# Kernel tuning notes

Hardware: AMD Instinct MI355X
Metric: run time of the kernel (lower is better)

## Reference

```python
import jax, jax.numpy as jnp
import numpy as np

S = 256      # pair sequence length (multiple of 32 -> no padding needed)
C = 128      # pair hidden dim
H = 4        # n_heads
D = 32       # head_dim
EPS = 1e-5
ENDING = False


def setup_inputs() -> dict:
    key = jax.random.key(0)
    ks = jax.random.split(key, 10)
    s = 0.02
    return {
        "x": jax.random.normal(ks[0], (1, S, S, C), dtype=jnp.float32),
        "ln_w": jnp.ones((C,), dtype=jnp.float32),
        "ln_b": jnp.zeros((C,), dtype=jnp.float32),
        "w_bias": jax.random.normal(ks[1], (H, C), dtype=jnp.float32) * s,   # linear.weight
        "w_q": jax.random.normal(ks[2], (H * D, C), dtype=jnp.float32) * s,  # linear_q.weight
        "w_k": jax.random.normal(ks[3], (H * D, C), dtype=jnp.float32) * s,
        "w_v": jax.random.normal(ks[4], (H * D, C), dtype=jnp.float32) * s,
        "w_g": jax.random.normal(ks[5], (H * D, C), dtype=jnp.float32) * s,  # linear_g.weight
        "w_o": jax.random.normal(ks[6], (C, H * D), dtype=jnp.float32) * s,  # linear_o.weight
    }


def reference(x, ln_w, ln_b, w_bias, w_q, w_k, w_v, w_g, w_o):
    h = x[0]  # [S, S, C]
    if ENDING:
        h = jnp.transpose(h, (1, 0, 2))
    # LayerNorm over channel dim
    mu = jnp.mean(h, axis=-1, keepdims=True)
    var = jnp.mean(jnp.square(h - mu), axis=-1, keepdims=True)
    h = (h - mu) * jax.lax.rsqrt(var + EPS) * ln_w + ln_b

    # pair-derived additive bias: [H, S, S], broadcast over the row (batch) dim
    tri_bias = jnp.einsum("ijc,hc->hij", h, w_bias)

    # per-head Q/K/V: weights are [H*D, C] with head-major rows
    wq = w_q.reshape(H, D, C)
    wk = w_k.reshape(H, D, C)
    wv = w_v.reshape(H, D, C)
    q = jnp.einsum("ijc,hdc->hijd", h, wq)  # [H, S(row), S(seq), D]
    k = jnp.einsum("ijc,hdc->hijd", h, wk)
    v = jnp.einsum("ijc,hdc->hijd", h, wv)

    scale = D ** -0.5
    # scores[h, i, j, k] = scale * q[h,i,j]\cdot k[h,i,k] + bias[h, j, k]
    scores = jnp.einsum("hijd,hikd->hijk", q, k) * scale + tri_bias[:, None, :, :]
    attn = jax.nn.softmax(scores, axis=-1)
    o = jnp.einsum("hijk,hikd->hijd", attn, v)          # [H, S, S, D]
    o = jnp.transpose(o, (1, 2, 0, 3)).reshape(S, S, H * D)

    # sigmoid gating and output projection
    g = jax.nn.sigmoid(jnp.einsum("ijc,ec->ije", h, w_g))
    out = jnp.einsum("ije,ce->ijc", o * g, w_o)          # [S, S, C]
    if ENDING:
        out = jnp.transpose(out, (1, 0, 2))
    return out[None]  # [1, S, S, C]
```

## Files before the change

kernel.cpp:

```cpp
#include <hip/hip_runtime.h>
#include <hip/hip_bf16.h>
#include <math.h>

#define SS 256
#define CC 128
#define NH 4
#define HD 32
#define M_TOT (SS*SS)
#define HEAD_STRIDE (M_TOT*HD)
#define PSTR 72
#define SCALE 0.17677669529663687f
#define QSCL 0.25507602861154995f
#define LOG2E 1.4426950408889634f

typedef short short8 __attribute__((ext_vector_type(8)));
typedef float f32x4 __attribute__((ext_vector_type(4)));
typedef unsigned short ushort_t;

static __device__ __forceinline__ unsigned int f2bf(float f) {
  unsigned int u = __builtin_bit_cast(unsigned int, f);
  u += 0x7fffu + ((u >> 16) & 1u);
  return u >> 16;
}
static __device__ __forceinline__ float bf2f(unsigned short b) {
  unsigned int u = ((unsigned int)b) << 16;
  return __builtin_bit_cast(float, u);
}

static __device__ __forceinline__ void async_copy16(const void* g, void* l) {
  __builtin_amdgcn_global_load_lds(
      (const __attribute__((address_space(1))) unsigned int*)g,
      (__attribute__((address_space(3))) unsigned int*)l, 16, 0, 0);
}

__global__ __launch_bounds__(256) void ln_kernel(
    const float* __restrict__ x, const float* __restrict__ ln_w,
    const float* __restrict__ ln_b, ushort_t* __restrict__ hbf) {
  int t = threadIdx.x;
  int row = blockIdx.x*8 + (t >> 5);
  int l = t & 31;
  float4 v = *(const float4*)&x[(size_t)row*CC + l*4];
  float s  = v.x + v.y + v.z + v.w;
  float s2 = v.x*v.x + v.y*v.y + v.z*v.z + v.w*v.w;
  #pragma unroll
  for (int o = 16; o > 0; o >>= 1) {
    s  += __shfl_xor(s, o);
    s2 += __shfl_xor(s2, o);
  }
  float mu  = s * (1.0f/CC);
  float var = s2 * (1.0f/CC) - mu*mu;
  float r = rsqrtf(var + 1e-5f);
  float4 w4 = *(const float4*)&ln_w[l*4];
  float4 b4 = *(const float4*)&ln_b[l*4];
  ushort4 o4;
  o4.x = (ushort_t)f2bf((v.x - mu) * r * w4.x + b4.x);
  o4.y = (ushort_t)f2bf((v.y - mu) * r * w4.y + b4.y);
  o4.z = (ushort_t)f2bf((v.z - mu) * r * w4.z + b4.z);
  o4.w = (ushort_t)f2bf((v.w - mu) * r * w4.w + b4.w);
  *(ushort4*)&hbf[(size_t)row*CC + l*4] = o4;
}

__global__ __launch_bounds__(256) void pack_w(
    const float* __restrict__ wq, const float* __restrict__ wk,
    const float* __restrict__ wv, const float* __restrict__ wg,
    const float* __restrict__ wb, const float* __restrict__ wo,
    ushort_t* __restrict__ wcomb, ushort_t* __restrict__ wbias,
    ushort_t* __restrict__ wobf) {
  int idx = blockIdx.x*256 + threadIdx.x;
  if (idx >= 656*128) return;
  int n = idx >> 7, kk = idx & 127;
  if (n < 512) {
    float val;
    if (n < 128)      val = wq[n*128 + kk];
    else if (n < 256) val = wk[(n-128)*128 + kk];
    else if (n < 384) val = wv[(n-256)*128 + kk];
    else              val = wg[(n-384)*128 + kk];
    wcomb[idx] = (ushort_t)f2bf(val);
  } else if (n < 528) {
    int r = n - 512;
    wbias[r*128 + kk] = (r < NH) ? (ushort_t)f2bf(wb[r*128 + kk] * LOG2E) : (ushort_t)0;
  } else {
    int r = n - 528;
    wobf[r*128 + kk] = (ushort_t)f2bf(wo[r*128 + kk]);
  }
}

__global__ __launch_bounds__(256, 3) void proj_mfma(
    const ushort_t* __restrict__ hbf, const ushort_t* __restrict__ wcomb,
    const ushort_t* __restrict__ wbias,
    ushort_t* __restrict__ qb, ushort_t* __restrict__ kb,
    ushort_t* __restrict__ vb, ushort_t* __restrict__ gbf,
    float* __restrict__ biasF) {
  __shared__ ushort_t Bsh[128*128];
  int mbase = blockIdx.x * 128;
  int sec = blockIdx.y;
  int tid = threadIdx.x;
  int wvi = tid >> 6, lane = tid & 63;
  int quad = lane >> 4, l15 = lane & 15;

  {
    int lrow4 = lane >> 4;
    int cl = lane & 15;
    #pragma unroll
    for (int t = 0; t < 8; t++) {
      int inst = wvi*8 + t;
      int row = inst*4 + lrow4;
      int gc = cl ^ (row & 7);
      async_copy16(wcomb + (size_t)(sec*128 + row)*128 + gc*8, Bsh + inst*512);
    }
  }
  __syncthreads();

  int wrow = (wvi >> 1) * 64, wcol = (wvi & 1) * 64;
  const f32x4 fz = {0.f,0.f,0.f,0.f};
  f32x4 acc[4][4];
  #pragma unroll
  for (int a = 0; a < 4; a++)
    #pragma unroll
    for (int b = 0; b < 4; b++) acc[a][b] = fz;

  #pragma unroll
  for (int s = 0; s < 4; s++) {
    short8 Af[4], Bf[4];
    #pragma unroll
    for (int f = 0; f < 4; f++) {
      int ra = mbase + wrow + f*16 + l15;
      Af[f] = *(const short8*)&hbf[(size_t)ra*128 + s*32 + quad*8];
      int rb = wcol + f*16 + l15;
      Bf[f] = *(const short8*)&Bsh[rb*128 + (((s*4+quad) ^ (rb&7)) << 3)];
    }
    #pragma unroll
    for (int mi = 0; mi < 4; mi++)
      #pragma unroll
      for (int ni = 0; ni < 4; ni++)
        acc[mi][ni] = __builtin_amdgcn_mfma_f32_16x16x32_bf16(Af[mi], Bf[ni], acc[mi][ni], 0, 0, 0);
  }

  #pragma unroll
  for (int mi = 0; mi < 4; mi++) {
    #pragma unroll
    for (int r = 0; r < 4; r++) {
      int m = mbase + wrow + mi*16 + quad*4 + r;
      #pragma unroll
      for (int ni = 0; ni < 4; ni++) {
        int n = wcol + ni*16 + l15;
        float v = acc[mi][ni][r];
        if (sec == 0) {
          qb[(size_t)(n>>5)*HEAD_STRIDE + (size_t)m*HD + (n&31)] = (ushort_t)f2bf(v * QSCL);
        } else if (sec == 1) {
          kb[(size_t)(n>>5)*HEAD_STRIDE + (size_t)m*HD + (n&31)] = (ushort_t)f2bf(v);
        } else if (sec == 2) {
          vb[(size_t)(n>>5)*HEAD_STRIDE + (size_t)m*HD + (n&31)] = (ushort_t)f2bf(v);
        } else {
          gbf[(size_t)m*CC + n] = (ushort_t)f2bf(1.0f/(1.0f + __expf(-v)));
        }
      }
    }
  }

  if (sec == 0) {
    short8 wbF[4];
    #pragma unroll
    for (int s = 0; s < 4; s++)
      wbF[s] = *(const short8*)&wbias[l15*128 + s*32 + quad*8];
    #pragma unroll
    for (int t2 = 0; t2 < 2; t2++) {
      int f2 = wvi*2 + t2;
      f32x4 bacc = fz;
      #pragma unroll
      for (int s = 0; s < 4; s++) {
        short8 Af = *(const short8*)&hbf[(size_t)(mbase + f2*16 + l15)*128 + s*32 + quad*8];
        bacc = __builtin_amdgcn_mfma_f32_16x16x32_bf16(wbF[s], Af, bacc, 0, 0, 0);
      }
      if (quad == 0) {
        int m = mbase + f2*16 + l15;
        int ji = m >> 8, ki = m & 255;
        int jt = ji >> 4, q2 = (ji >> 2) & 3, rg = ji & 3;
        int kt = ki >> 4, lf = ki & 15;
        #pragma unroll
        for (int r = 0; r < 4; r++)
          biasF[(size_t)(((r*16 + jt)*16 + kt) << 8) + (q2*16 + lf)*4 + rg] = bacc[r];
      }
    }
  }
}

__global__ __launch_bounds__(256, 3) void attn_mfma(
    const ushort_t* __restrict__ qb, const ushort_t* __restrict__ kb,
    const ushort_t* __restrict__ vb, const float* __restrict__ biasF,
    const ushort_t* __restrict__ gbf, ushort_t* __restrict__ ogated) {
  __shared__ ushort_t Vt[32*256];
  __shared__ ushort_t Pb[4*64*PSTR];
  int i = blockIdx.x, hh = blockIdx.y;
  int tid = threadIdx.x;
  int wvi = tid >> 6, lane = tid & 63;
  int quad = lane >> 4, l15 = lane & 15;

  {
    const ushort_t* vrow = vb + ((size_t)hh*M_TOT + (size_t)i*SS + tid) * HD;
    const uint4* v4 = (const uint4*)vrow;
    int cs = tid >> 3, ce = tid & 7;
    #pragma unroll
    for (int c = 0; c < 4; c++) {
      uint4 r = v4[c];
      unsigned int u[4] = {r.x, r.y, r.z, r.w};
      #pragma unroll
      for (int w = 0; w < 4; w++) {
        int d = c*8 + w*2;
        Vt[d*256     + ((cs ^ (d&7))     << 3) + ce] = (ushort_t)(u[w] & 0xffffu);
        Vt[(d+1)*256 + ((cs ^ ((d+1)&7)) << 3) + ce] = (ushort_t)(u[w] >> 16);
      }
    }
  }

  const ushort_t* qbase = qb + ((size_t)hh*M_TOT + (size_t)i*SS + wvi*64) * HD;
  short8 Qf[4];
  #pragma unroll
  for (int a = 0; a < 4; a++)
    Qf[a] = *(const short8*)(qbase + (a*16 + l15)*HD + quad*8);

  const ushort_t* kbp = kb + ((size_t)hh*M_TOT + (size_t)i*SS) * HD;
  const float* bb = biasF + (size_t)(hh*16 + wvi*4) * 4096;

  const f32x4 fz = {0.f, 0.f, 0.f, 0.f};
  f32x4 Oa[4][2];
  #pragma unroll
  for (int a = 0; a < 4; a++) { Oa[a][0] = fz; Oa[a][1] = fz; }
  float lsum[4][4] = {};

  ushort_t* pw = Pb + wvi*64*PSTR;

  __syncthreads();

  #pragma unroll
  for (int it = 0; it < 4; it++) {
    #pragma unroll
    for (int b = 0; b < 4; b++) {
      int kt = it*4 + b;
      short8 Kf = *(const short8*)(kbp + (kt*16 + l15)*HD + quad*8);
      #pragma unroll
      for (int a = 0; a < 4; a++) {
        float4 bt = *(const float4*)(bb + (size_t)((a*16 + kt) << 8) + lane*4);
        f32x4 bias4 = {bt.x, bt.y, bt.z, bt.w};
        f32x4 S = __builtin_amdgcn_mfma_f32_16x16x32_bf16(Qf[a], Kf, bias4, 0, 0, 0);
        float p0 = __builtin_amdgcn_exp2f(S[0]);
        float p1 = __builtin_amdgcn_exp2f(S[1]);
        float p2 = __builtin_amdgcn_exp2f(S[2]);
        float p3 = __builtin_amdgcn_exp2f(S[3]);
        lsum[a][0] += p0; lsum[a][1] += p1; lsum[a][2] += p2; lsum[a][3] += p3;
        ushort_t* pwa = pw + (a*16 + quad*4)*PSTR + b*16 + l15;
        pwa[0*PSTR] = (ushort_t)f2bf(p0);
        pwa[1*PSTR] = (ushort_t)f2bf(p1);
        pwa[2*PSTR] = (ushort_t)f2bf(p2);
        pwa[3*PSTR] = (ushort_t)f2bf(p3);
      }
    }
    #pragma unroll
    for (int kk = 0; kk < 2; kk++) {
      int cb = it*8 + kk*4;
      int sw = ((cb + quad) ^ (l15 & 7)) << 3;
      short8 Vf0 = *(const short8*)&Vt[l15*256 + sw];
      short8 Vf1 = *(const short8*)&Vt[(16 + l15)*256 + sw];
      #pragma unroll
      for (int a = 0; a < 4; a++) {
        short8 Pf = *(const short8*)&pw[(a*16 + l15)*PSTR + kk*32 + quad*8];
        Oa[a][0] = __builtin_amdgcn_mfma_f32_16x16x32_bf16(Pf, Vf0, Oa[a][0], 0, 0, 0);
        Oa[a][1] = __builtin_amdgcn_mfma_f32_16x16x32_bf16(Pf, Vf1, Oa[a][1], 0, 0, 0);
      }
    }
  }

  float linv[4][4];
  #pragma unroll
  for (int a = 0; a < 4; a++) {
    #pragma unroll
    for (int r = 0; r < 4; r++) {
      float v = lsum[a][r];
      v += __shfl_xor(v, 1);
      v += __shfl_xor(v, 2);
      v += __shfl_xor(v, 4);
      v += __shfl_xor(v, 8);
      linv[a][r] = 1.0f / v;
    }
  }
  const ushort_t* gp = gbf + ((size_t)i*SS + wvi*64)*CC + hh*HD;
  ushort_t* ob = ogated + ((size_t)i*SS + wvi*64)*CC + hh*HD;
  #pragma unroll
  for (int a = 0; a < 4; a++) {
    #pragma unroll
    for (int r = 0; r < 4; r++) {
      int row = (a*16 + quad*4 + r) * CC;
      float g0 = bf2f(gp[row + l15]);
      float g1 = bf2f(gp[row + 16 + l15]);
      ob[row + l15]      = (ushort_t)f2bf(Oa[a][0][r] * linv[a][r] * g0);
      ob[row + 16 + l15] = (ushort_t)f2bf(Oa[a][1][r] * linv[a][r] * g1);
    }
  }
}

__global__ __launch_bounds__(256, 3) void out_mfma(
    const ushort_t* __restrict__ ogated, const ushort_t* __restrict__ wobf,
    float* __restrict__ out) {
  __shared__ ushort_t Bsh[128*128];
  int mbase = blockIdx.x * 128;
  int tid = threadIdx.x;
  int wvi = tid >> 6, lane = tid & 63;
  int quad = lane >> 4, l15 = lane & 15;

  {
    int lrow4 = lane >> 4;
    int cl = lane & 15;
    #pragma unroll
    for (int t = 0; t < 8; t++) {
      int inst = wvi*8 + t;
      int row = inst*4 + lrow4;
      int gc = cl ^ (row & 7);
      async_copy16(wobf + (size_t)row*128 + gc*8, Bsh + inst*512);
    }
  }
  __syncthreads();

  int wrow = (wvi >> 1) * 64, wcol = (wvi & 1) * 64;
  const f32x4 fz = {0.f,0.f,0.f,0.f};
  f32x4 acc[4][4];
  #pragma unroll
  for (int a = 0; a < 4; a++)
    #pragma unroll
    for (int b = 0; b < 4; b++) acc[a][b] = fz;

  #pragma unroll
  for (int s = 0; s < 4; s++) {
    short8 Af[4], Bf[4];
    #pragma unroll
    for (int f = 0; f < 4; f++) {
      int ra = mbase + wrow + f*16 + l15;
      Af[f] = *(const short8*)&ogated[(size_t)ra*128 + s*32 + quad*8];
      int rb = wcol + f*16 + l15;
      Bf[f] = *(const short8*)&Bsh[rb*128 + (((s*4+quad) ^ (rb&7)) << 3)];
    }
    #pragma unroll
    for (int mi = 0; mi < 4; mi++)
      #pragma unroll
      for (int ni = 0; ni < 4; ni++)
        acc[mi][ni] = __builtin_amdgcn_mfma_f32_16x16x32_bf16(Af[mi], Bf[ni], acc[mi][ni], 0, 0, 0);
  }

  #pragma unroll
  for (int mi = 0; mi < 4; mi++) {
    #pragma unroll
    for (int r = 0; r < 4; r++) {
      int m = mbase + wrow + mi*16 + quad*4 + r;
      #pragma unroll
      for (int ni = 0; ni < 4; ni++) {
        int n = wcol + ni*16 + l15;
        out[(size_t)m*CC + n] = acc[mi][ni][r];
      }
    }
  }
}

extern "C" void kernel_launch(void* const* d_in, const int* in_sizes, int n_in,
                              void* d_out, int out_size, void* d_ws, size_t ws_size,
                              hipStream_t stream) {
  const float* x    = (const float*)d_in[0];
  const float* ln_w = (const float*)d_in[1];
  const float* ln_b = (const float*)d_in[2];
  const float* w_bias = (const float*)d_in[3];
  const float* w_q  = (const float*)d_in[4];
  const float* w_k  = (const float*)d_in[5];
  const float* w_v  = (const float*)d_in[6];
  const float* w_g  = (const float*)d_in[7];
  const float* w_o  = (const float*)d_in[8];
  float* out = (float*)d_out;

  char* B = (char*)d_ws;
  ushort_t* hbf   = (ushort_t*)(B + 0);
  ushort_t* qb    = (ushort_t*)(B + 16777216);
  ushort_t* kb    = (ushort_t*)(B + 33554432);
  ushort_t* vb    = (ushort_t*)(B + 50331648);
  ushort_t* gbf   = (ushort_t*)(B + 67108864);
  float*    biasF = (float*)   (B + 83886080);
  ushort_t* wcomb = (ushort_t*)(B + 84934656);
  ushort_t* wbias = (ushort_t*)(B + 85065728);
  ushort_t* wobf  = (ushort_t*)(B + 85069824);
  ushort_t* ogated = hbf;

  ln_kernel<<<M_TOT/8, 256, 0, stream>>>(x, ln_w, ln_b, hbf);
  pack_w<<<(656*128 + 255)/256, 256, 0, stream>>>(w_q, w_k, w_v, w_g, w_bias, w_o,
                                                  wcomb, wbias, wobf);
  proj_mfma<<<dim3(M_TOT/128, 4), 256, 0, stream>>>(hbf, wcomb, wbias,
                                                    qb, kb, vb, gbf, biasF);
  attn_mfma<<<dim3(SS, NH), 256, 0, stream>>>(qb, kb, vb, biasF, gbf, ogated);
  out_mfma<<<M_TOT/128, 256, 0, stream>>>(ogated, wobf, out);
}
```

Measured before the change: 187.9 us.

## Fuse LayerNorm into projection kernel and loop over weight sections per block

Removes the separate LayerNorm kernel. The projection kernel now normalizes its 128-row tile of x straight into swizzled LDS as bf16, and each block loops over the four weight sections (Q, K, V, G), so the A tile is read once into registers and reused. This avoids writing and re-reading the bf16 normalized activations through global memory, and avoids the four-fold re-read of A across grid.y. In exchange there are fewer blocks, LDS use doubles, launch bounds drop to 2 waves per SIMD, and the per-section weight reloads are serialized with barriers.

```diff
diff --git a/kernel.cpp b/kernel.cpp
--- a/kernel.cpp
+++ b/kernel.cpp
@@ -31,33 +31,6 @@
   __builtin_amdgcn_global_load_lds(
       (const __attribute__((address_space(1))) unsigned int*)g,
       (__attribute__((address_space(3))) unsigned int*)l, 16, 0, 0);
-}
-
-__global__ __launch_bounds__(256) void ln_kernel(
-    const float* __restrict__ x, const float* __restrict__ ln_w,
-    const float* __restrict__ ln_b, ushort_t* __restrict__ hbf) {
-  int t = threadIdx.x;
-  int row = blockIdx.x*8 + (t >> 5);
-  int l = t & 31;
-  float4 v = *(const float4*)&x[(size_t)row*CC + l*4];
-  float s  = v.x + v.y + v.z + v.w;
-  float s2 = v.x*v.x + v.y*v.y + v.z*v.z + v.w*v.w;
-  #pragma unroll
-  for (int o = 16; o > 0; o >>= 1) {
-    s  += __shfl_xor(s, o);
-    s2 += __shfl_xor(s2, o);
-  }
-  float mu  = s * (1.0f/CC);
-  float var = s2 * (1.0f/CC) - mu*mu;
-  float r = rsqrtf(var + 1e-5f);
-  float4 w4 = *(const float4*)&ln_w[l*4];
-  float4 b4 = *(const float4*)&ln_b[l*4];
-  ushort4 o4;
-  o4.x = (ushort_t)f2bf((v.x - mu) * r * w4.x + b4.x);
-  o4.y = (ushort_t)f2bf((v.y - mu) * r * w4.y + b4.y);
-  o4.z = (ushort_t)f2bf((v.z - mu) * r * w4.z + b4.z);
-  o4.w = (ushort_t)f2bf((v.w - mu) * r * w4.w + b4.w);
-  *(ushort4*)&hbf[(size_t)row*CC + l*4] = o4;
 }
 
 __global__ __launch_bounds__(256) void pack_w(
@@ -85,103 +58,157 @@
   }
 }
 
-__global__ __launch_bounds__(256, 3) void proj_mfma(
-    const ushort_t* __restrict__ hbf, const ushort_t* __restrict__ wcomb,
+__global__ __launch_bounds__(256, 2) void fused_proj(
+    const float* __restrict__ x, const float* __restrict__ ln_w,
+    const float* __restrict__ ln_b, const ushort_t* __restrict__ wcomb,
     const ushort_t* __restrict__ wbias,
     ushort_t* __restrict__ qb, ushort_t* __restrict__ kb,
     ushort_t* __restrict__ vb, ushort_t* __restrict__ gbf,
     float* __restrict__ biasF) {
+  __shared__ ushort_t Ash[128*128];
   __shared__ ushort_t Bsh[128*128];
   int mbase = blockIdx.x * 128;
-  int sec = blockIdx.y;
   int tid = threadIdx.x;
   int wvi = tid >> 6, lane = tid & 63;
   int quad = lane >> 4, l15 = lane & 15;
+  int lrow4 = lane >> 4;
+  int cl = lane & 15;
+
+  #pragma unroll
+  for (int t = 0; t < 8; t++) {
+    int inst = wvi*8 + t;
+    int row = inst*4 + lrow4;
+    int gc = cl ^ (row & 7);
+    async_copy16(wcomb + (size_t)row*128 + gc*8, Bsh + inst*512);
+  }
 
   {
-    int lrow4 = lane >> 4;
-    int cl = lane & 15;
-    #pragma unroll
-    for (int t = 0; t < 8; t++) {
-      int inst = wvi*8 + t;
-      int row = inst*4 + lrow4;
-      int gc = cl ^ (row & 7);
-      async_copy16(wcomb + (size_t)(sec*128 + row)*128 + gc*8, Bsh + inst*512);
+    int l = tid & 31;
+    int rsub = tid >> 5;
+    float4 w4 = *(const float4*)&ln_w[l*4];
+    float4 b4 = *(const float4*)&ln_b[l*4];
+    #pragma unroll
+    for (int pass = 0; pass < 16; pass++) {
+      int row = pass*8 + rsub;
+      float4 v = *(const float4*)&x[(size_t)(mbase + row)*CC + l*4];
+      float s  = v.x + v.y + v.z + v.w;
+      float s2 = v.x*v.x + v.y*v.y + v.z*v.z + v.w*v.w;
+      #pragma unroll
+      for (int o = 16; o > 0; o >>= 1) {
+        s  += __shfl_xor(s, o);
+        s2 += __shfl_xor(s2, o);
+      }
+      float mu  = s * (1.0f/CC);
+      float var = s2 * (1.0f/CC) - mu*mu;
+      float r = rsqrtf(var + 1e-5f);
+      ushort4 o4;
+      o4.x = (ushort_t)f2bf((v.x - mu) * r * w4.x + b4.x);
+      o4.y = (ushort_t)f2bf((v.y - mu) * r * w4.y + b4.y);
+      o4.z = (ushort_t)f2bf((v.z - mu) * r * w4.z + b4.z);
+      o4.w = (ushort_t)f2bf((v.w - mu) * r * w4.w + b4.w);
+      int addr = row*128 + (((l >> 1) ^ (row & 7)) << 3) + (l & 1)*4;
+      *(ushort4*)&Ash[addr] = o4;
     }
   }
   __syncthreads();
 
   int wrow = (wvi >> 1) * 64, wcol = (wvi & 1) * 64;
   const f32x4 fz = {0.f,0.f,0.f,0.f};
-  f32x4 acc[4][4];
-  #pragma unroll
-  for (int a = 0; a < 4; a++)
-    #pragma unroll
-    for (int b = 0; b < 4; b++) acc[a][b] = fz;
-
-  #pragma unroll
-  for (int s = 0; s < 4; s++) {
-    short8 Af[4], Bf[4];
+
+  short8 Afr[4][4];
+  #pragma unroll
+  for (int s = 0; s < 4; s++)
     #pragma unroll
     for (int f = 0; f < 4; f++) {
-      int ra = mbase + wrow + f*16 + l15;
-      Af[f] = *(const short8*)&hbf[(size_t)ra*128 + s*32 + quad*8];
-      int rb = wcol + f*16 + l15;
-      Bf[f] = *(const short8*)&Bsh[rb*128 + (((s*4+quad) ^ (rb&7)) << 3)];
-    }
-    #pragma unroll
-    for (int mi = 0; mi < 4; mi++)
-      #pragma unroll
-      for (int ni = 0; ni < 4; ni++)
-        acc[mi][ni] = __builtin_amdgcn_mfma_f32_16x16x32_bf16(Af[mi], Bf[ni], acc[mi][ni], 0, 0, 0);
-  }
-
-  #pragma unroll
-  for (int mi = 0; mi < 4; mi++) {
-    #pragma unroll
-    for (int r = 0; r < 4; r++) {
-      int m = mbase + wrow + mi*16 + quad*4 + r;
-      #pragma unroll
-      for (int ni = 0; ni < 4; ni++) {
-        int n = wcol + ni*16 + l15;
-        float v = acc[mi][ni][r];
-        if (sec == 0) {
-          qb[(size_t)(n>>5)*HEAD_STRIDE + (size_t)m*HD + (n&31)] = (ushort_t)f2bf(v * QSCL);
-        } else if (sec == 1) {
-          kb[(size_t)(n>>5)*HEAD_STRIDE + (size_t)m*HD + (n&31)] = (ushort_t)f2bf(v);
-        } else if (sec == 2) {
-          vb[(size_t)(n>>5)*HEAD_STRIDE + (size_t)m*HD + (n&31)] = (ushort_t)f2bf(v);
-        } else {
-          gbf[(size_t)m*CC + n] = (ushort_t)f2bf(1.0f/(1.0f + __expf(-v)));
+      int ra = wrow + f*16 + l15;
+      Afr[s][f] = *(const short8*)&Ash[ra*128 + (((s*4+quad) ^ (ra&7)) << 3)];
+    }
+
+  #pragma unroll
+  for (int sec = 0; sec < 4; sec++) {
+    f32x4 acc[4][4];
+    #pragma unroll
+    for (int a = 0; a < 4; a++)
+      #pragma unroll
+      for (int b = 0; b < 4; b++) acc[a][b] = fz;
+
+    #pragma unroll
+    for (int s = 0; s < 4; s++) {
+      short8 Bf[4];
+      #pragma unroll
+      for (int f = 0; f < 4; f++) {
+        int rb = wcol + f*16 + l15;
+        Bf[f] = *(const short8*)&Bsh[rb*128 + (((s*4+quad) ^ (rb&7)) << 3)];
+      }
+      #pragma unroll
+      for (int mi = 0; mi < 4; mi++)
+        #pragma unroll
+        for (int ni = 0; ni < 4; ni++)
+          acc[mi][ni] = __builtin_amdgcn_mfma_f32_16x16x32_bf16(Afr[s][mi], Bf[ni], acc[mi][ni], 0, 0, 0);
+    }
+
+    __syncthreads();
+
+    if (sec < 3) {
+      #pragma unroll
+      for (int t = 0; t < 8; t++) {
+        int inst = wvi*8 + t;
+        int row = inst*4 + lrow4;
+        int gc = cl ^ (row & 7);
+        async_copy16(wcomb + (size_t)((sec+1)*128 + row)*128 + gc*8, Bsh + inst*512);
+      }
+    }
+
+    #pragma unroll
+    for (int mi = 0; mi < 4; mi++) {
+      #pragma unroll
+      for (int r = 0; r < 4; r++) {
+        int m = mbase + wrow + mi*16 + quad*4 + r;
+        #pragma unroll
+        for (int ni = 0; ni < 4; ni++) {
+          int n = wcol + ni*16 + l15;
+          float v = acc[mi][ni][r];
+          if (sec == 0) {
+            qb[(size_t)(n>>5)*HEAD_STRIDE + (size_t)m*HD + (n&31)] = (ushort_t)f2bf(v * QSCL);
+          } else if (sec == 1) {
+            kb[(size_t)(n>>5)*HEAD_STRIDE + (size_t)m*HD + (n&31)] = (ushort_t)f2bf(v);
+          } else if (sec == 2) {
+            vb[(size_t)(n>>5)*HEAD_STRIDE + (size_t)m*HD + (n&31)] = (ushort_t)f2bf(v);
+          } else {
+            gbf[(size_t)m*CC + n] = (ushort_t)f2bf(1.0f/(1.0f + __expf(-v)));
+          }
         }
       }
     }
-  }
-
-  if (sec == 0) {
-    short8 wbF[4];
-    #pragma unroll
-    for (int s = 0; s < 4; s++)
-      wbF[s] = *(const short8*)&wbias[l15*128 + s*32 + quad*8];
-    #pragma unroll
-    for (int t2 = 0; t2 < 2; t2++) {
-      int f2 = wvi*2 + t2;
-      f32x4 bacc = fz;
-      #pragma unroll
-      for (int s = 0; s < 4; s++) {
-        short8 Af = *(const short8*)&hbf[(size_t)(mbase + f2*16 + l15)*128 + s*32 + quad*8];
-        bacc = __builtin_amdgcn_mfma_f32_16x16x32_bf16(wbF[s], Af, bacc, 0, 0, 0);
-      }
-      if (quad == 0) {
-        int m = mbase + f2*16 + l15;
-        int ji = m >> 8, ki = m & 255;
-        int jt = ji >> 4, q2 = (ji >> 2) & 3, rg = ji & 3;
-        int kt = ki >> 4, lf = ki & 15;
+
+    if (sec == 0) {
+      short8 wbF[4];
+      #pragma unroll
+      for (int s = 0; s < 4; s++)
+        wbF[s] = *(const short8*)&wbias[l15*128 + s*32 + quad*8];
+      #pragma unroll
+      for (int t2 = 0; t2 < 2; t2++) {
+        int f2 = wvi*2 + t2;
+        f32x4 bacc = fz;
         #pragma unroll
-        for (int r = 0; r < 4; r++)
-          biasF[(size_t)(((r*16 + jt)*16 + kt) << 8) + (q2*16 + lf)*4 + rg] = bacc[r];
-      }
-    }
+        for (int s = 0; s < 4; s++) {
+          int ra = f2*16 + l15;
+          short8 Af = *(const short8*)&Ash[ra*128 + (((s*4+quad) ^ (ra&7)) << 3)];
+          bacc = __builtin_amdgcn_mfma_f32_16x16x32_bf16(wbF[s], Af, bacc, 0, 0, 0);
+        }
+        if (quad == 0) {
+          int m = mbase + f2*16 + l15;
+          int ji = m >> 8, ki = m & 255;
+          int jt = ji >> 4, q2 = (ji >> 2) & 3, rg = ji & 3;
+          int kt = ki >> 4, lf = ki & 15;
+          #pragma unroll
+          for (int r = 0; r < 4; r++)
+            biasF[(size_t)(((r*16 + jt)*16 + kt) << 8) + (q2*16 + lf)*4 + rg] = bacc[r];
+        }
+      }
+    }
+
+    if (sec < 3) __syncthreads();
   }
 }
 
@@ -374,7 +401,7 @@
   float* out = (float*)d_out;
 
   char* B = (char*)d_ws;
-  ushort_t* hbf   = (ushort_t*)(B + 0);
+  ushort_t* ogated = (ushort_t*)(B + 0);
   ushort_t* qb    = (ushort_t*)(B + 16777216);
   ushort_t* kb    = (ushort_t*)(B + 33554432);
   ushort_t* vb    = (ushort_t*)(B + 50331648);
@@ -383,13 +410,11 @@
   ushort_t* wcomb = (ushort_t*)(B + 84934656);
   ushort_t* wbias = (ushort_t*)(B + 85065728);
   ushort_t* wobf  = (ushort_t*)(B + 85069824);
-  ushort_t* ogated = hbf;
-
-  ln_kernel<<<M_TOT/8, 256, 0, stream>>>(x, ln_w, ln_b, hbf);
+
   pack_w<<<(656*128 + 255)/256, 256, 0, stream>>>(w_q, w_k, w_v, w_g, w_bias, w_o,
                                                   wcomb, wbias, wobf);
-  proj_mfma<<<dim3(M_TOT/128, 4), 256, 0, stream>>>(hbf, wcomb, wbias,
-                                                    qb, kb, vb, gbf, biasF);
+  fused_proj<<<M_TOT/128, 256, 0, stream>>>(x, ln_w, ln_b, wcomb, wbias,
+                                            qb, kb, vb, gbf, biasF);
   attn_mfma<<<dim3(SS, NH), 256, 0, stream>>>(qb, kb, vb, biasF, gbf, ogated);
   out_mfma<<<M_TOT/128, 256, 0, stream>>>(ogated, wobf, out);
 }
```

Result: faster. 166.1 us (-11.6%).
